# Optimization experiments

Hardware: AMD Instinct MI355X
Metric: run time of the kernel (lower is better)

The kernel has to match this reference:

```python
import jax, jax.numpy as jnp
import numpy as np
import math

E = 1024      # embed_dim
H = 16        # num_heads
D = 32        # head_dim = E // H // 2
DEPTH = 12
LAMBDA_INIT = 0.8 - 0.6 * math.exp(-0.3 * DEPTH)
B, T = 4, 1024
EPS = 1e-5


def setup_inputs() -> dict:
    key = jax.random.key(0)
    ks = jax.random.split(key, 10)
    s = 0.02  # realistic init scale for weight matrices
    return {
        "x": jax.random.normal(ks[0], (B, T, E), jnp.float32),
        "Wq": jax.random.normal(ks[1], (E, E), jnp.float32) * s,
        "Wk": jax.random.normal(ks[2], (E, E), jnp.float32) * s,
        "Wv": jax.random.normal(ks[3], (E, E), jnp.float32) * s,
        "Wo": jax.random.normal(ks[4], (E, E), jnp.float32) * s,
        "lambda_q1": jax.random.normal(ks[5], (D,), jnp.float32) * 0.1,
        "lambda_k1": jax.random.normal(ks[6], (D,), jnp.float32) * 0.1,
        "lambda_q2": jax.random.normal(ks[7], (D,), jnp.float32) * 0.1,
        "lambda_k2": jax.random.normal(ks[8], (D,), jnp.float32) * 0.1,
        "g": jnp.ones((2 * D,), jnp.float32),  # subln affine weight
    }


def reference(x, Wq, Wk, Wv, Wo, lambda_q1, lambda_k1, lambda_q2, lambda_k2, g):
    b, t, _ = x.shape
    scaling = D ** -0.5
    # projections (torch Linear: x @ W.T), split into 2H half-width q/k heads
    q = (x @ Wq.T).reshape(b, t, 2 * H, D).transpose(0, 2, 1, 3) * scaling  # [b,2H,t,D]
    k = (x @ Wk.T).reshape(b, t, 2 * H, D).transpose(0, 2, 1, 3)            # [b,2H,t,D]
    v = (x @ Wv.T).reshape(b, t, H, 2 * D).transpose(0, 2, 1, 3)            # [b,H,t,2D]
    # dual score maps, fp32 softmax
    aw = jnp.einsum('bhqd,bhkd->bhqk', q, k)               # [b,2H,t,t]
    aw = jnp.nan_to_num(aw)
    aw = jax.nn.softmax(aw.astype(jnp.float32), axis=-1).astype(q.dtype)
    # scalar lambda
    lam1 = jnp.exp(jnp.sum(lambda_q1 * lambda_k1))
    lam2 = jnp.exp(jnp.sum(lambda_q2 * lambda_k2))
    lam = lam1 - lam2 + LAMBDA_INIT
    # differential subtract of the paired softmax maps
    aw = aw.reshape(b, H, 2, t, t)
    aw = aw[:, :, 0] - lam * aw[:, :, 1]                   # [b,H,t,t]
    attn = jnp.einsum('bhqk,bhkd->bhqd', aw, v)            # [b,H,t,2D]
    # per-head RMSNorm over 2D channel dim (affine)
    attn = attn * jax.lax.rsqrt(jnp.mean(attn * attn, axis=-1, keepdims=True) + EPS) * g
    attn = attn * (1.0 - LAMBDA_INIT)
    attn = attn.transpose(0, 2, 1, 3).reshape(b, t, H * 2 * D)  # [b,t,E]
    return attn @ Wo.T
```

## Files before the change

kernel.cpp:

```cpp
#include <hip/hip_runtime.h>
#include <math.h>

#define E_   1024
#define H_   16
#define B_   4
#define T_   1024
#define LAMBDA_INIT 0.783605766532f
#define SCALE_QL2E 0.25503486f

typedef short s16x8 __attribute__((ext_vector_type(8)));
typedef float f32x4 __attribute__((ext_vector_type(4)));

#define SWZ(c, r) ((((c) ^ ((r) & 7)) * 8))

__device__ inline ushort f2bf(float x) {
    unsigned u = __builtin_bit_cast(unsigned, x);
    u += 0x7fffu + ((u >> 16) & 1u);
    return (ushort)(u >> 16);
}

__device__ inline uint f2bf2(float lo, float hi) {
#if __has_builtin(__builtin_amdgcn_cvt_pk_bf16_f32)
    typedef __bf16 bf16x2_t __attribute__((ext_vector_type(2)));
    bf16x2_t r = __builtin_amdgcn_cvt_pk_bf16_f32(lo, hi);
    return __builtin_bit_cast(uint, r);
#else
    uint ul = __builtin_bit_cast(uint, lo);
    uint uh = __builtin_bit_cast(uint, hi);
    ul += 0x7fffu + ((ul >> 16) & 1u);
    uh += 0x7fffu + ((uh >> 16) & 1u);
    return __builtin_amdgcn_perm(uh, ul, 0x07060302u);
#endif
}

__device__ inline float exp2fast(float x) {
#if __has_builtin(__builtin_amdgcn_exp2f)
    return __builtin_amdgcn_exp2f(x);
#else
    return exp2f(x);
#endif
}

__device__ inline void gl_lds16(const ushort* g, ushort* l) {
    __builtin_amdgcn_global_load_lds((const __attribute__((address_space(1))) void*)g,
                                     (__attribute__((address_space(3))) void*)l,
                                     16, 0, 0);
}

__global__ __launch_bounds__(256) void prep(
    const float* __restrict__ x,  const float* __restrict__ Wq,
    const float* __restrict__ Wk, const float* __restrict__ Wv,
    const float* __restrict__ Wo,
    const float* __restrict__ lq1, const float* __restrict__ lk1,
    const float* __restrict__ lq2, const float* __restrict__ lk2,
    ushort* __restrict__ xb, ushort* __restrict__ Wqb, ushort* __restrict__ Wkb,
    ushort* __restrict__ Wvb, ushort* __restrict__ Wob, float* __restrict__ lamp)
{
    const int blk = blockIdx.x;
    const int tid = threadIdx.x;
    if (blk >= 4096) {
        if (tid < 64) {
            float p1 = 0.f, p2 = 0.f;
            if (tid < 32) { p1 = lq1[tid] * lk1[tid]; p2 = lq2[tid] * lk2[tid]; }
            #pragma unroll
            for (int off = 32; off; off >>= 1) {
                p1 += __shfl_xor(p1, off);
                p2 += __shfl_xor(p2, off);
            }
            if (tid == 0) lamp[0] = expf(p1) - expf(p2) + LAMBDA_INIT;
        }
        return;
    }
    const float* in;
    ushort* out;
    int base;
    if (blk < 2048) { in = x; out = xb; base = blk; }
    else {
        int t = blk - 2048, w = t >> 9;
        base = t & 511;
        in  = w == 0 ? Wq  : (w == 1 ? Wk  : (w == 2 ? Wv  : Wo));
        out = w == 0 ? Wqb : (w == 1 ? Wkb : (w == 2 ? Wvb : Wob));
    }
    int i = (base * 256 + tid) * 8;
    float4 a = *(const float4*)&in[i];
    float4 b = *(const float4*)&in[i + 4];
    union { ushort u[8]; uint4 v; } o;
    o.u[0] = f2bf(a.x); o.u[1] = f2bf(a.y); o.u[2] = f2bf(a.z); o.u[3] = f2bf(a.w);
    o.u[4] = f2bf(b.x); o.u[5] = f2bf(b.y); o.u[6] = f2bf(b.z); o.u[7] = f2bf(b.w);
    *(uint4*)&out[i] = o.v;
}

__global__ __launch_bounds__(256) void gemm_qkv(
    const ushort* __restrict__ Xb, const ushort* __restrict__ Wqb,
    const ushort* __restrict__ Wkb, const ushort* __restrict__ Wvb,
    ushort* __restrict__ QK, ushort* __restrict__ Vt)
{
    __shared__ __align__(16) ushort As[128 * 64];
    __shared__ __align__(16) ushort Ws[128 * 64];
    const int tid = threadIdx.x;
    const int wave = tid >> 6, lane = tid & 63;
    const int l15 = lane & 15, quad = lane >> 4;
    const int bm = blockIdx.y * 128;
    const int bng = blockIdx.x * 128;
    const int region = bng >> 10;
    const ushort* W = region == 0 ? Wqb : (region == 1 ? Wkb : Wvb);
    const float scale = region == 0 ? SCALE_QL2E : 1.0f;
    const int wn = bng & 1023;
    const int lr  = lane >> 3;
    const int jsw = ((lane & 7) ^ lr) * 8;
    const int roff0 = l15 * 64 + SWZ(quad, l15);
    const int roff1 = l15 * 64 + SWZ(4 + quad, l15);

    f32x4 acc[4][4] = {};
    const int wr = wave >> 1, wc = wave & 1;

    for (int k0 = 0; k0 < 1024; k0 += 64) {
        #pragma unroll
        for (int p = 0; p < 4; ++p) {
            int r = wave * 32 + p * 8;
            gl_lds16(&Xb[(size_t)(bm + r + lr) * 1024 + k0 + jsw], &As[r * 64]);
            gl_lds16(&W [(size_t)(wn + r + lr) * 1024 + k0 + jsw], &Ws[r * 64]);
        }
        __syncthreads();
        #pragma unroll
        for (int ks = 0; ks < 2; ++ks) {
            const int roff = ks ? roff1 : roff0;
            s16x8 a[4], b[4];
            #pragma unroll
            for (int i = 0; i < 4; ++i)
                a[i] = *(const s16x8*)&As[(wr * 64 + i * 16) * 64 + roff];
            #pragma unroll
            for (int j = 0; j < 4; ++j)
                b[j] = *(const s16x8*)&Ws[(wc * 64 + j * 16) * 64 + roff];
            if (region < 2) {
                #pragma unroll
                for (int i = 0; i < 4; ++i)
                    #pragma unroll
                    for (int j = 0; j < 4; ++j)
                        acc[i][j] = __builtin_amdgcn_mfma_f32_16x16x32_bf16(b[j], a[i], acc[i][j], 0, 0, 0);
            } else {
                #pragma unroll
                for (int i = 0; i < 4; ++i)
                    #pragma unroll
                    for (int j = 0; j < 4; ++j)
                        acc[i][j] = __builtin_amdgcn_mfma_f32_16x16x32_bf16(a[i], b[j], acc[i][j], 0, 0, 0);
            }
        }
        __syncthreads();
    }

    if (region < 2) {
        #pragma unroll
        for (int i = 0; i < 4; ++i) {
            int row = bm + wr * 64 + i * 16 + l15;
            #pragma unroll
            for (int j = 0; j < 4; ++j) {
                int col = region * 1024 + wn + wc * 64 + j * 16 + quad * 4;
                ushort4 o;
                o.x = f2bf(acc[i][j][0] * scale); o.y = f2bf(acc[i][j][1] * scale);
                o.z = f2bf(acc[i][j][2] * scale); o.w = f2bf(acc[i][j][3] * scale);
                *(ushort4*)&QK[(size_t)row * 2048 + col] = o;
            }
        }
    } else {
        const int bb = bm >> 10;
        const int t0 = (bm & 1023) + wr * 64 + quad * 4;
        #pragma unroll
        for (int i = 0; i < 4; ++i)
            #pragma unroll
            for (int j = 0; j < 4; ++j) {
                int e = wn + wc * 64 + j * 16 + l15;
                ushort4 o;
                o.x = f2bf(acc[i][j][0]); o.y = f2bf(acc[i][j][1]);
                o.z = f2bf(acc[i][j][2]); o.w = f2bf(acc[i][j][3]);
                *(ushort4*)&Vt[((size_t)bb * E_ + e) * T_ + t0 + i * 16] = o;
            }
    }
}

__global__ __launch_bounds__(256) void gemm_out(
    const ushort* __restrict__ Ab, const ushort* __restrict__ Wob,
    float* __restrict__ C)
{
    __shared__ __align__(16) ushort As[64 * 64];
    __shared__ __align__(16) ushort Ws[64 * 64];
    const int tid = threadIdx.x;
    const int wave = tid >> 6, lane = tid & 63;
    const int l15 = lane & 15, quad = lane >> 4;
    const int bm = blockIdx.y * 64;
    const int bn = blockIdx.x * 64;
    const int lr  = lane >> 3;
    const int jsw = ((lane & 7) ^ lr) * 8;
    const int roff0 = l15 * 64 + SWZ(quad, l15);
    const int roff1 = l15 * 64 + SWZ(4 + quad, l15);

    f32x4 acc[2][2] = {};
    const int wr = wave >> 1, wc = wave & 1;

    for (int k0 = 0; k0 < 1024; k0 += 64) {
        #pragma unroll
        for (int p = 0; p < 2; ++p) {
            int r = wave * 16 + p * 8;
            gl_lds16(&Ab[(size_t)(bm + r + lr) * 1024 + k0 + jsw], &As[r * 64]);
            gl_lds16(&Wob[(size_t)(bn + r + lr) * 1024 + k0 + jsw], &Ws[r * 64]);
        }
        __syncthreads();
        #pragma unroll
        for (int ks = 0; ks < 2; ++ks) {
            const int roff = ks ? roff1 : roff0;
            s16x8 a[2], b[2];
            #pragma unroll
            for (int i = 0; i < 2; ++i)
                a[i] = *(const s16x8*)&As[(wr * 32 + i * 16) * 64 + roff];
            #pragma unroll
            for (int j = 0; j < 2; ++j)
                b[j] = *(const s16x8*)&Ws[(wc * 32 + j * 16) * 64 + roff];
            #pragma unroll
            for (int i = 0; i < 2; ++i)
                #pragma unroll
                for (int j = 0; j < 2; ++j)
                    acc[i][j] = __builtin_amdgcn_mfma_f32_16x16x32_bf16(b[j], a[i], acc[i][j], 0, 0, 0);
        }
        __syncthreads();
    }

    #pragma unroll
    for (int i = 0; i < 2; ++i) {
        int row = bm + wr * 32 + i * 16 + l15;
        #pragma unroll
        for (int j = 0; j < 2; ++j) {
            int col = bn + wc * 32 + j * 16 + quad * 4;
            float4 o;
            o.x = acc[i][j][0]; o.y = acc[i][j][1];
            o.z = acc[i][j][2]; o.w = acc[i][j][3];
            *(float4*)&C[(size_t)row * 1024 + col] = o;
        }
    }
}

__global__ __launch_bounds__(256, 4) void diff_attn(
    const ushort* __restrict__ QK, const ushort* __restrict__ Vt,
    const float* __restrict__ g, const float* __restrict__ lamp,
    ushort* __restrict__ O)
{
    __shared__ __align__(16) ushort Ks[2][4096];
    __shared__ __align__(16) ushort Vts[2][4096];
    __shared__ __align__(16) ushort Pt[4][1024];

    const int tid  = threadIdx.x;
    const int lane = tid & 63;
    const int wave = tid >> 6;
    const int l15  = lane & 15;
    const int quad = lane >> 4;

    const int blk = blockIdx.x;
    const int bh = blk & 63;
    const int qt = blk >> 6;
    const int b  = bh >> 4;
    const int h  = bh & 15;
    const int q0 = qt * 64;
    const int hoff = h * 64;
    const size_t rowbase = (size_t)b * T_;

    const ushort* Qg = QK;
    const ushort* Kg = QK + 1024;
    const size_t vtbase = ((size_t)b * E_ + hoff) * T_;

    const int lr  = lane >> 3;
    const int jsw = ((lane & 7) ^ lr) * 8;

    const size_t qrow = (rowbase + q0 + wave * 16 + l15) * 2048 + hoff;
    s16x8 aq0 = *(const s16x8*)&Qg[qrow + quad * 8];
    s16x8 aq1 = *(const s16x8*)&Qg[qrow + 32 + quad * 8];

    const int kaoff0 = l15 * 64 + SWZ(quad,     l15);
    const int kaoff1 = l15 * 64 + SWZ(4 + quad, l15);
    ushort* myPt = &Pt[wave][0];

    const f32x4 zf = {0.f, 0.f, 0.f, 0.f};
    f32x4 o0[4] = {zf, zf, zf, zf};
    f32x4 o1[4] = {zf, zf, zf, zf};
    float lsum0 = 0.f, lsum1 = 0.f;

    #pragma unroll
    for (int p = 0; p < 2; ++p) {
        int r = wave * 16 + p * 8;
        gl_lds16(&Kg[(rowbase + r + lr) * 2048 + hoff + jsw], &Ks[0][r * 64]);
        gl_lds16(&Vt[vtbase + (size_t)(r + lr) * T_ + jsw],   &Vts[0][r * 64]);
    }
    __syncthreads();

    for (int kt = 0; kt < 16; ++kt) {
        const int cur = kt & 1;
        const int nxt = cur ^ 1;
        {
            const int ktn = (kt + 1) & 15;
            #pragma unroll
            for (int p = 0; p < 2; ++p) {
                int r = wave * 16 + p * 8;
                gl_lds16(&Kg[(rowbase + ktn * 64 + r + lr) * 2048 + hoff + jsw],
                         &Ks[nxt][r * 64]);
                gl_lds16(&Vt[vtbase + (size_t)(r + lr) * T_ + ktn * 64 + jsw],
                         &Vts[nxt][r * 64]);
            }
        }

        s16x8 va[4][2];
        #pragma unroll
        for (int jt = 0; jt < 4; ++jt) {
            va[jt][0] = *(const s16x8*)&Vts[cur][jt * 1024 + kaoff0];
            va[jt][1] = *(const s16x8*)&Vts[cur][jt * 1024 + kaoff1];
        }

        {
            f32x4 S[4];
            #pragma unroll
            for (int jk = 0; jk < 4; ++jk) {
                s16x8 ka = *(const s16x8*)&Ks[cur][jk * 1024 + kaoff0];
                S[jk] = __builtin_amdgcn_mfma_f32_16x16x32_bf16(ka, aq0, zf, 0, 0, 0);
            }
            #pragma unroll
            for (int jk = 0; jk < 4; ++jk) {
                float e0 = exp2fast(S[jk][0]), e1 = exp2fast(S[jk][1]);
                float e2 = exp2fast(S[jk][2]), e3 = exp2fast(S[jk][3]);
                lsum0 += (e0 + e1) + (e2 + e3);
                uint2 pk; pk.x = f2bf2(e0, e1); pk.y = f2bf2(e2, e3);
                *(uint2*)&myPt[l15 * 64 + SWZ(2 * jk + (quad >> 1), l15) + (quad & 1) * 4] = pk;
            }
            #pragma unroll
            for (int h2 = 0; h2 < 2; ++h2) {
                s16x8 pf = *(const s16x8*)&myPt[h2 ? kaoff1 : kaoff0];
                #pragma unroll
                for (int jt = 0; jt < 4; ++jt)
                    o0[jt] = __builtin_amdgcn_mfma_f32_16x16x32_bf16(va[jt][h2], pf, o0[jt], 0, 0, 0);
            }
        }
        {
            f32x4 S[4];
            #pragma unroll
            for (int jk = 0; jk < 4; ++jk) {
                s16x8 ka = *(const s16x8*)&Ks[cur][jk * 1024 + kaoff1];
                S[jk] = __builtin_amdgcn_mfma_f32_16x16x32_bf16(ka, aq1, zf, 0, 0, 0);
            }
            #pragma unroll
            for (int jk = 0; jk < 4; ++jk) {
                float e0 = exp2fast(S[jk][0]), e1 = exp2fast(S[jk][1]);
                float e2 = exp2fast(S[jk][2]), e3 = exp2fast(S[jk][3]);
                lsum1 += (e0 + e1) + (e2 + e3);
                uint2 pk; pk.x = f2bf2(e0, e1); pk.y = f2bf2(e2, e3);
                *(uint2*)&myPt[l15 * 64 + SWZ(2 * jk + (quad >> 1), l15) + (quad & 1) * 4] = pk;
            }
            #pragma unroll
            for (int h2 = 0; h2 < 2; ++h2) {
                s16x8 pf = *(const s16x8*)&myPt[h2 ? kaoff1 : kaoff0];
                #pragma unroll
                for (int jt = 0; jt < 4; ++jt)
                    o1[jt] = __builtin_amdgcn_mfma_f32_16x16x32_bf16(va[jt][h2], pf, o1[jt], 0, 0, 0);
            }
        }
        __syncthreads();
    }

    lsum0 += __shfl_xor(lsum0, 16); lsum0 += __shfl_xor(lsum0, 32);
    lsum1 += __shfl_xor(lsum1, 16); lsum1 += __shfl_xor(lsum1, 32);

    const float lam = lamp[0];
    const float fin = 1.f - LAMBDA_INIT;
    float i0 = 1.f / lsum0;
    float i1 = lam / lsum1;
    float val[4][4];
    float ssq = 0.f;
    #pragma unroll
    for (int jt = 0; jt < 4; ++jt)
        #pragma unroll
        for (int r = 0; r < 4; ++r) {
            float v = o0[jt][r] * i0 - o1[jt][r] * i1;
            val[jt][r] = v;
            ssq += v * v;
        }
    ssq += __shfl_xor(ssq, 16);
    ssq += __shfl_xor(ssq, 32);
    float sc = rsqrtf(ssq * (1.f / 64.f) + 1e-5f) * fin;
    size_t rowoff = (rowbase + q0 + wave * 16 + l15) * 1024 + hoff;
    #pragma unroll
    for (int jt = 0; jt < 4; ++jt) {
        float4 gv = *(const float4*)&g[jt * 16 + quad * 4];
        uint p01 = f2bf2(val[jt][0] * sc * gv.x, val[jt][1] * sc * gv.y);
        uint p23 = f2bf2(val[jt][2] * sc * gv.z, val[jt][3] * sc * gv.w);
        *(uint*)&O[rowoff + jt * 16 + quad * 4 + 0] = p01;
        *(uint*)&O[rowoff + jt * 16 + quad * 4 + 2] = p23;
    }
}

extern "C" void kernel_launch(void* const* d_in, const int* in_sizes, int n_in,
                              void* d_out, int out_size, void* d_ws, size_t ws_size,
                              hipStream_t stream)
{
    const float* x   = (const float*)d_in[0];
    const float* Wq  = (const float*)d_in[1];
    const float* Wk  = (const float*)d_in[2];
    const float* Wv  = (const float*)d_in[3];
    const float* Wo  = (const float*)d_in[4];
    const float* lq1 = (const float*)d_in[5];
    const float* lk1 = (const float*)d_in[6];
    const float* lq2 = (const float*)d_in[7];
    const float* lk2 = (const float*)d_in[8];
    const float* g   = (const float*)d_in[9];
    float* out = (float*)d_out;

    const int M = B_ * T_;
    const size_t ME = (size_t)M * E_;
    const size_t EE = (size_t)E_ * E_;
    ushort* xb  = (ushort*)d_ws;
    ushort* Wqb = xb  + ME;
    ushort* Wkb = Wqb + EE;
    ushort* Wvb = Wkb + EE;
    ushort* Wob = Wvb + EE;
    ushort* QK  = Wob + EE;
    ushort* Vtb = QK + (size_t)M * 2048;
    float*  lamp = (float*)(Vtb + ME);
    ushort* Ab  = xb;

    prep<<<4097, 256, 0, stream>>>(x, Wq, Wk, Wv, Wo, lq1, lk1, lq2, lk2,
                                   xb, Wqb, Wkb, Wvb, Wob, lamp);
    gemm_qkv<<<dim3(24, 32), 256, 0, stream>>>(xb, Wqb, Wkb, Wvb, QK, Vtb);
    diff_attn<<<B_ * H_ * (T_ / 64), 256, 0, stream>>>(QK, Vtb, g, lamp, Ab);
    gemm_out<<<dim3(16, 64), 256, 0, stream>>>(Ab, Wob, out);
}
```

Baseline: 193.7 us.

## Double-buffer LDS tiles in QKV and output GEMMs to overlap loads with MFMA

Both projection GEMMs now keep two LDS buffers per operand. The next K-tile is issued with direct global-to-LDS loads before computing on the current one, and a partial vmcnt wait gates the barrier. The aim is to hide global-load latency behind the MFMA work instead of stalling on a full sync each iteration. The cost is doubled LDS use per block, which may reduce occupancy, plus hand-managed waitcnt counts that must match the number of outstanding loads.

```diff
diff --git a/kernel.cpp b/kernel.cpp
--- a/kernel.cpp
+++ b/kernel.cpp
@@ -90,13 +90,64 @@
     *(uint4*)&out[i] = o.v;
 }
 
+#define QKV_STAGE(NXTB, KN)                                                     \
+    {                                                                           \
+        _Pragma("unroll")                                                       \
+        for (int p = 0; p < 4; ++p) {                                           \
+            int r = wave * 32 + p * 8;                                          \
+            gl_lds16(&Xb[(size_t)(bm + r + lr) * 1024 + (KN) + jsw], &As[NXTB][r * 64]); \
+            gl_lds16(&W [(size_t)(wn + r + lr) * 1024 + (KN) + jsw], &Ws[NXTB][r * 64]); \
+        }                                                                       \
+    }
+
+#define QKV_COMPUTE(CURB)                                                       \
+    {                                                                           \
+        _Pragma("unroll")                                                       \
+        for (int ks = 0; ks < 2; ++ks) {                                        \
+            const int roff = ks ? roff1 : roff0;                                \
+            s16x8 a[4], b[4];                                                   \
+            _Pragma("unroll")                                                   \
+            for (int i = 0; i < 4; ++i)                                         \
+                a[i] = *(const s16x8*)&As[CURB][(wr * 64 + i * 16) * 64 + roff];\
+            _Pragma("unroll")                                                   \
+            for (int j = 0; j < 4; ++j)                                         \
+                b[j] = *(const s16x8*)&Ws[CURB][(wc * 64 + j * 16) * 64 + roff];\
+            if (region < 2) {                                                   \
+                _Pragma("unroll")                                               \
+                for (int i = 0; i < 4; ++i)                                     \
+                    _Pragma("unroll")                                           \
+                    for (int j = 0; j < 4; ++j)                                 \
+                        acc[i][j] = __builtin_amdgcn_mfma_f32_16x16x32_bf16(b[j], a[i], acc[i][j], 0, 0, 0); \
+            } else {                                                            \
+                _Pragma("unroll")                                               \
+                for (int i = 0; i < 4; ++i)                                     \
+                    _Pragma("unroll")                                           \
+                    for (int j = 0; j < 4; ++j)                                 \
+                        acc[i][j] = __builtin_amdgcn_mfma_f32_16x16x32_bf16(a[i], b[j], acc[i][j], 0, 0, 0); \
+            }                                                                   \
+        }                                                                       \
+    }
+
+#define QKV_STEP(CURB, NXTB, KT)                                                \
+    {                                                                           \
+        if ((KT) != 15) {                                                       \
+            QKV_STAGE(NXTB, ((KT) + 1) * 64);                                   \
+            asm volatile("s_waitcnt vmcnt(8)" ::: "memory");                    \
+        } else {                                                                \
+            asm volatile("s_waitcnt vmcnt(0)" ::: "memory");                    \
+        }                                                                       \
+        __builtin_amdgcn_s_barrier();                                           \
+        QKV_COMPUTE(CURB);                                                      \
+        if ((KT) != 15) __builtin_amdgcn_s_barrier();                           \
+    }
+
 __global__ __launch_bounds__(256) void gemm_qkv(
     const ushort* __restrict__ Xb, const ushort* __restrict__ Wqb,
     const ushort* __restrict__ Wkb, const ushort* __restrict__ Wvb,
     ushort* __restrict__ QK, ushort* __restrict__ Vt)
 {
-    __shared__ __align__(16) ushort As[128 * 64];
-    __shared__ __align__(16) ushort Ws[128 * 64];
+    __shared__ __align__(16) ushort As[2][128 * 64];
+    __shared__ __align__(16) ushort Ws[2][128 * 64];
     const int tid = threadIdx.x;
     const int wave = tid >> 6, lane = tid & 63;
     const int l15 = lane & 15, quad = lane >> 4;
@@ -114,39 +165,11 @@
     f32x4 acc[4][4] = {};
     const int wr = wave >> 1, wc = wave & 1;
 
-    for (int k0 = 0; k0 < 1024; k0 += 64) {
-        #pragma unroll
-        for (int p = 0; p < 4; ++p) {
-            int r = wave * 32 + p * 8;
-            gl_lds16(&Xb[(size_t)(bm + r + lr) * 1024 + k0 + jsw], &As[r * 64]);
-            gl_lds16(&W [(size_t)(wn + r + lr) * 1024 + k0 + jsw], &Ws[r * 64]);
-        }
-        __syncthreads();
-        #pragma unroll
-        for (int ks = 0; ks < 2; ++ks) {
-            const int roff = ks ? roff1 : roff0;
-            s16x8 a[4], b[4];
-            #pragma unroll
-            for (int i = 0; i < 4; ++i)
-                a[i] = *(const s16x8*)&As[(wr * 64 + i * 16) * 64 + roff];
-            #pragma unroll
-            for (int j = 0; j < 4; ++j)
-                b[j] = *(const s16x8*)&Ws[(wc * 64 + j * 16) * 64 + roff];
-            if (region < 2) {
-                #pragma unroll
-                for (int i = 0; i < 4; ++i)
-                    #pragma unroll
-                    for (int j = 0; j < 4; ++j)
-                        acc[i][j] = __builtin_amdgcn_mfma_f32_16x16x32_bf16(b[j], a[i], acc[i][j], 0, 0, 0);
-            } else {
-                #pragma unroll
-                for (int i = 0; i < 4; ++i)
-                    #pragma unroll
-                    for (int j = 0; j < 4; ++j)
-                        acc[i][j] = __builtin_amdgcn_mfma_f32_16x16x32_bf16(a[i], b[j], acc[i][j], 0, 0, 0);
-            }
-        }
-        __syncthreads();
+    QKV_STAGE(0, 0);
+
+    for (int kt2 = 0; kt2 < 16; kt2 += 2) {
+        QKV_STEP(0, 1, kt2);
+        QKV_STEP(1, 0, kt2 + 1);
     }
 
     if (region < 2) {
@@ -178,12 +201,55 @@
     }
 }
 
+#define OUT_STAGE(NXTB, KN)                                                     \
+    {                                                                           \
+        _Pragma("unroll")                                                       \
+        for (int p = 0; p < 2; ++p) {                                           \
+            int r = wave * 16 + p * 8;                                          \
+            gl_lds16(&Ab[(size_t)(bm + r + lr) * 1024 + (KN) + jsw], &As[NXTB][r * 64]);  \
+            gl_lds16(&Wob[(size_t)(bn + r + lr) * 1024 + (KN) + jsw], &Ws[NXTB][r * 64]); \
+        }                                                                       \
+    }
+
+#define OUT_COMPUTE(CURB)                                                       \
+    {                                                                           \
+        _Pragma("unroll")                                                       \
+        for (int ks = 0; ks < 2; ++ks) {                                        \
+            const int roff = ks ? roff1 : roff0;                                \
+            s16x8 a[2], b[2];                                                   \
+            _Pragma("unroll")                                                   \
+            for (int i = 0; i < 2; ++i)                                         \
+                a[i] = *(const s16x8*)&As[CURB][(wr * 32 + i * 16) * 64 + roff];\
+            _Pragma("unroll")                                                   \
+            for (int j = 0; j < 2; ++j)                                         \
+                b[j] = *(const s16x8*)&Ws[CURB][(wc * 32 + j * 16) * 64 + roff];\
+            _Pragma("unroll")                                                   \
+            for (int i = 0; i < 2; ++i)                                         \
+                _Pragma("unroll")                                               \
+                for (int j = 0; j < 2; ++j)                                     \
+                    acc[i][j] = __builtin_amdgcn_mfma_f32_16x16x32_bf16(b[j], a[i], acc[i][j], 0, 0, 0); \
+        }                                                                       \
+    }
+
+#define OUT_STEP(CURB, NXTB, KT)                                                \
+    {                                                                           \
+        if ((KT) != 15) {                                                       \
+            OUT_STAGE(NXTB, ((KT) + 1) * 64);                                   \
+            asm volatile("s_waitcnt vmcnt(4)" ::: "memory");                    \
+        } else {                                                                \
+            asm volatile("s_waitcnt vmcnt(0)" ::: "memory");                    \
+        }                                                                       \
+        __builtin_amdgcn_s_barrier();                                           \
+        OUT_COMPUTE(CURB);                                                      \
+        if ((KT) != 15) __builtin_amdgcn_s_barrier();                           \
+    }
+
 __global__ __launch_bounds__(256) void gemm_out(
     const ushort* __restrict__ Ab, const ushort* __restrict__ Wob,
     float* __restrict__ C)
 {
-    __shared__ __align__(16) ushort As[64 * 64];
-    __shared__ __align__(16) ushort Ws[64 * 64];
+    __shared__ __align__(16) ushort As[2][64 * 64];
+    __shared__ __align__(16) ushort Ws[2][64 * 64];
     const int tid = threadIdx.x;
     const int wave = tid >> 6, lane = tid & 63;
     const int l15 = lane & 15, quad = lane >> 4;
@@ -197,31 +263,11 @@
     f32x4 acc[2][2] = {};
     const int wr = wave >> 1, wc = wave & 1;
 
-    for (int k0 = 0; k0 < 1024; k0 += 64) {
-        #pragma unroll
-        for (int p = 0; p < 2; ++p) {
-            int r = wave * 16 + p * 8;
-            gl_lds16(&Ab[(size_t)(bm + r + lr) * 1024 + k0 + jsw], &As[r * 64]);
-            gl_lds16(&Wob[(size_t)(bn + r + lr) * 1024 + k0 + jsw], &Ws[r * 64]);
-        }
-        __syncthreads();
-        #pragma unroll
-        for (int ks = 0; ks < 2; ++ks) {
-            const int roff = ks ? roff1 : roff0;
-            s16x8 a[2], b[2];
-            #pragma unroll
-            for (int i = 0; i < 2; ++i)
-                a[i] = *(const s16x8*)&As[(wr * 32 + i * 16) * 64 + roff];
-            #pragma unroll
-            for (int j = 0; j < 2; ++j)
-                b[j] = *(const s16x8*)&Ws[(wc * 32 + j * 16) * 64 + roff];
-            #pragma unroll
-            for (int i = 0; i < 2; ++i)
-                #pragma unroll
-                for (int j = 0; j < 2; ++j)
-                    acc[i][j] = __builtin_amdgcn_mfma_f32_16x16x32_bf16(b[j], a[i], acc[i][j], 0, 0, 0);
-        }
-        __syncthreads();
+    OUT_STAGE(0, 0);
+
+    for (int kt2 = 0; kt2 < 16; kt2 += 2) {
+        OUT_STEP(0, 1, kt2);
+        OUT_STEP(1, 0, kt2 + 1);
     }
 
     #pragma unroll
```

Measured after the change: 189.5 us, median of 2. 2.2% less time.
